# Optimization experiments

Measured on AMD Instinct MI355X. Metric: run time of the kernel, lower is better.

Reference implementation:

```python
import jax, jax.numpy as jnp
import numpy as np
import math

H = 256; W = 256
NUM_CURVES = 256
NUM_SAMPLES = 32
NUM_BEZIERS = 2
BDEG = 5            # Bernstein degree used by the module (bezier_degree+1)
CTRL_STRIDE = 5     # bezier_degree+1; segments share endpoints, wrap (closed curve)
N_CTRL = NUM_BEZIERS * CTRL_STRIDE   # 10 control points per closed curve
PIX_CHUNK = 512
CHOLESKY_BOUND = jnp.array([0.5, 0.0, 0.5], jnp.float32)


def _bernstein():
    # t in linspace(0.007, 0.993, S) exactly as _update_bernstein_cache
    t = jnp.linspace(0.007, 0.993, NUM_SAMPLES)
    i = jnp.arange(BDEG + 1, dtype=jnp.float32)
    comb = jnp.array([math.comb(BDEG, k) for k in range(BDEG + 1)], jnp.float32)
    return comb * (t[:, None] ** i) * ((1.0 - t[:, None]) ** (BDEG - i))  # [S, BDEG+1]


def _render(control_points, features_dc, cholesky, opacity, depth, background):
    Bmat = _bernstein()
    # closed curve: segment k uses control points (k*5 + j) mod 10, j=0..5
    seg_idx = (jnp.arange(NUM_BEZIERS)[:, None] * CTRL_STRIDE
               + jnp.arange(BDEG + 1)[None, :]) % N_CTRL          # [K, 6]
    seg_ctrl = control_points[:, seg_idx]                          # [N, K, 6, 2]
    pts = jnp.einsum('sj,nkjd->nksd', Bmat, seg_ctrl)              # [N, K, S, 2]
    pts = pts.reshape(NUM_CURVES, -1, 2)                           # [N, Gper, 2]
    gper = pts.shape[1]

    # normalized [-1,1] -> pixel coords
    means = (jnp.tanh(pts) * 0.5 + 0.5) * jnp.array([W, H], jnp.float32)
    means = means.reshape(-1, 2)                                   # [G, 2]

    # 2x2 covariance from lower-triangular Cholesky (per curve)
    c = cholesky + CHOLESKY_BOUND[None, :]                         # l11, l21, l22
    s00 = c[:, 0] ** 2
    s01 = c[:, 0] * c[:, 1]
    s11 = c[:, 1] ** 2 + c[:, 2] ** 2
    det = s00 * s11 - s01 ** 2
    conic = jnp.stack([s11 / det, -s01 / det, s00 / det], -1)      # [N, 3]

    rep = lambda a: jnp.repeat(a, gper, axis=0)
    conic_g = rep(conic)                                           # [G, 3]
    color_g = rep(jax.nn.sigmoid(features_dc))                     # [G, 3]
    alpha_g = rep(jax.nn.sigmoid(opacity))[:, 0]                   # [G]
    depth_g = rep(depth)[:, 0]                                     # [G]

    order = jnp.argsort(depth_g)                                   # front-to-back
    means_s = means[order]
    conic_s = conic_g[order]
    color_s = color_g[order]
    alpha_s = alpha_g[order]

    ys, xs = jnp.meshgrid(jnp.arange(H, dtype=jnp.float32) + 0.5,
                          jnp.arange(W, dtype=jnp.float32) + 0.5, indexing='ij')
    pix = jnp.stack([xs.ravel(), ys.ravel()], -1).reshape(-1, PIX_CHUNK, 2)

    @jax.checkpoint
    def render_chunk(p):                                           # [C,2] -> [C,3]
        dx = p[:, None, 0] - means_s[None, :, 0]
        dy = p[:, None, 1] - means_s[None, :, 1]
        power = (-0.5 * (conic_s[None, :, 0] * dx * dx
                         + conic_s[None, :, 2] * dy * dy)
                 - conic_s[None, :, 1] * dx * dy)
        a = jnp.clip(alpha_s[None, :] * jnp.exp(power), 0.0, 0.999)
        logT = jnp.cumsum(jnp.log1p(-a), axis=1)
        t_excl = jnp.exp(logT - jnp.log1p(-a))   # transmittance before each splat
        rgb = (a * t_excl) @ color_s             # [C, 3]
        return rgb + jnp.exp(logT[:, -1:]) * background[None, :]

    img = jax.lax.map(render_chunk, pix)                           # [P/C, C, 3]
    return jnp.clip(img.reshape(H, W, 3), 0.0, 1.0)


def setup_inputs() -> dict:
    key = jax.random.key(0)
    k1, k2, k3, k4 = jax.random.split(key, 4)
    return {
        "control_points": jax.random.normal(k1, (NUM_CURVES, N_CTRL, 2), jnp.float32),
        "features_dc": jax.random.uniform(k2, (NUM_CURVES, 3), jnp.float32),
        "cholesky": jax.random.uniform(k3, (NUM_CURVES, 3), jnp.float32),
        "opacity": jnp.ones((NUM_CURVES, 1), jnp.float32),
        "depth": jax.random.uniform(k4, (NUM_CURVES, 1), jnp.float32),
        "background": jnp.ones((3,), jnp.float32),
    }


def reference(control_points, features_dc, cholesky, opacity, depth, background):
    return _render(control_points, features_dc, cholesky, opacity, depth, background)
```

## Files before the change

### kernel.cpp

```cpp
#include <hip/hip_runtime.h>
#include <hip/hip_fp16.h>
#include <math.h>

#define NCURVES   256
#define GPER      64
#define NUM_G     (NCURVES*GPER)
#define IMG_W     256
#define IMG_H     256
#define TILE      8
#define TILES_X   (IMG_W/TILE)
#define TILES_Y   (IMG_H/TILE)
#define NTILES    (TILES_X*TILES_Y)
#define REC_F     8

#define A_MIN     3.0e-6f
#define P_CUT     (-12.6f)
#define T_EPS     1.0e-5f

#define WQ        4
#define GQ        (NUM_G/WQ)

__global__ __launch_bounds__(GPER)
void prep(const float* __restrict__ ctrl,
          const float* __restrict__ features,
          const float* __restrict__ cholesky,
          const float* __restrict__ opacity,
          const float* __restrict__ depth,
          float*       __restrict__ recs,
          unsigned*    __restrict__ bbox)
{
    int c   = blockIdx.x;
    int tid = threadIdx.x;

    float dc = depth[c];
    int r = 0;
    #pragma unroll
    for (int jj = 0; jj < 4; ++jj) {
        int j = tid + jj*64;
        float dj = depth[j];
        r += (dj < dc) || (dj == dc && j < c);
    }
    #pragma unroll
    for (int off = 32; off > 0; off >>= 1) r += __shfl_down(r, off, 64);
    r = __shfl(r, 0, 64);

    float c0 = cholesky[3*c+0] + 0.5f;
    float c1 = cholesky[3*c+1];
    float c2 = cholesky[3*c+2] + 0.5f;
    float s00 = c0*c0;
    float s01 = c0*c1;
    float s11 = c1*c1 + c2*c2;
    float inv = 1.0f / (s00*s11 - s01*s01);
    float A  =  s11*inv;
    float Bc = -s01*inv;
    float Cc =  s00*inv;

    float cr = 1.0f/(1.0f + __expf(-features[3*c+0]));
    float cg = 1.0f/(1.0f + __expf(-features[3*c+1]));
    float cb = 1.0f/(1.0f + __expf(-features[3*c+2]));
    float al = 1.0f/(1.0f + __expf(-opacity[c]));

    float cut = fmaxf(2.0f*(__logf(al) - __logf(A_MIN)), 0.0f);
    float rx = sqrtf(cut * s00);
    float ry = sqrtf(cut * s11);

    int k = tid >> 5;
    int s = tid & 31;
    float t = 0.007f + (float)s * (0.986f/31.0f);
    float u = 1.0f - t;
    float t2=t*t, t3=t2*t, t4=t3*t, t5=t4*t;
    float u2=u*u, u3=u2*u, u4=u3*u, u5=u4*u;
    float w[6] = { u5, 5.0f*t*u4, 10.0f*t2*u3, 10.0f*t3*u2, 5.0f*t4*u, t5 };

    const float* cp = ctrl + c*20;
    float px = 0.0f, py = 0.0f;
    #pragma unroll
    for (int j = 0; j < 6; ++j) {
        int idx = (k*5 + j) % 10;
        px += w[j]*cp[2*idx+0];
        py += w[j]*cp[2*idx+1];
    }
    float mx = (tanhf(px)*0.5f + 0.5f) * (float)IMG_W;
    float my = (tanhf(py)*0.5f + 0.5f) * (float)IMG_H;

    int gi = r*GPER + tid;

    unsigned rg  = (unsigned)__half_as_ushort(__float2half_rn(cr))
                 | ((unsigned)__half_as_ushort(__float2half_rn(cg)) << 16);
    unsigned cbp = (unsigned)__half_as_ushort(__float2half_rn(cb));

    float4* o4 = (float4*)(recs + (size_t)gi*REC_F);
    o4[0] = make_float4(mx, my, A, Bc);
    o4[1] = make_float4(Cc, al, __uint_as_float(rg), __uint_as_float(cbp));

    int tx0 = min(max((int)floorf((mx - rx) * (1.0f/TILE)), 0), TILES_X-1);
    int tx1 = min(max((int)floorf((mx + rx) * (1.0f/TILE)), 0), TILES_X-1);
    int ty0 = min(max((int)floorf((my - ry) * (1.0f/TILE)), 0), TILES_Y-1);
    int ty1 = min(max((int)floorf((my + ry) * (1.0f/TILE)), 0), TILES_Y-1);
    bbox[gi] = (unsigned)tx0 | ((unsigned)ty0<<8) | ((unsigned)tx1<<16) | ((unsigned)ty1<<24);
}

__global__ __launch_bounds__(256)
void render8x8(const float*    __restrict__ recs,
               const unsigned* __restrict__ bbox,
               const float*    __restrict__ background,
               float*          __restrict__ out)
{
    __shared__ unsigned short lst[WQ][GQ];
    __shared__ float4         pc[WQ][64];

    int tid   = threadIdx.x;
    int lane  = tid & 63;
    int w     = tid >> 6;
    int tile  = blockIdx.x;
    int tilex = tile & (TILES_X-1);
    int tiley = tile >> 5;
    unsigned long long lmask = (1ull << lane) - 1ull;

    int gb = w * GQ;

    int cnt = 0;
    #pragma unroll 1
    for (int b = 0; b < 8; ++b) {
        unsigned bb[8];
        #pragma unroll
        for (int u = 0; u < 8; ++u)
            bb[u] = bbox[gb + (b*8 + u)*64 + lane];
        #pragma unroll
        for (int u = 0; u < 8; ++u) {
            unsigned v = bb[u];
            bool pred = (tilex >= (int)( v        & 0xff)) &
                        (tilex <= (int)((v >> 16) & 0xff)) &
                        (tiley >= (int)((v >>  8) & 0xff)) &
                        (tiley <= (int)((v >> 24) & 0xff));
            unsigned long long m = __ballot(pred ? 1 : 0);
            if (pred)
                lst[w][cnt + (int)__popcll(m & lmask)] =
                    (unsigned short)((b*8 + u)*64 + lane);
            cnt += (int)__popcll(m);
        }
    }

    float pxf = (float)(tilex*TILE + (lane & 7)) + 0.5f;
    float pyf = (float)(tiley*TILE + (lane >> 3)) + 0.5f;

    float T = 1.0f, accr = 0.0f, accg = 0.0f, accb = 0.0f;

    #pragma unroll 2
    for (int j = 0; j < cnt; ++j) {
        int g = gb + (int)lst[w][j];
        const float4* rp = (const float4*)(recs + (size_t)g*REC_F);
        float4 r0 = rp[0];
        float4 r1 = rp[1];
        float dx = pxf - r0.x;
        float dy = pyf - r0.y;
        float p  = -0.5f*(r0.z*dx*dx + r1.x*dy*dy) - r0.w*dx*dy;
        if (p > P_CUT) {
            float a = fminf(r1.y * __expf(p), 0.999f);
            float wgt = a * T;
            unsigned rg = __float_as_uint(r1.z);
            accr += wgt * __half2float(__ushort_as_half((unsigned short)(rg & 0xffff)));
            accg += wgt * __half2float(__ushort_as_half((unsigned short)(rg >> 16)));
            accb += wgt * __half2float(__ushort_as_half((unsigned short)__float_as_uint(r1.w)));
            T *= (1.0f - a);
        }
        if (!__any(T > T_EPS)) break;
    }

    pc[w][lane] = make_float4(accr, accg, accb, T);
    __syncthreads();

    if (w == 0) {
        float4 a0 = pc[0][lane];
        float4 a1 = pc[1][lane];
        float4 a2 = pc[2][lane];
        float4 a3 = pc[3][lane];
        float r = a0.x + a0.w*(a1.x + a1.w*(a2.x + a2.w*a3.x));
        float g = a0.y + a0.w*(a1.y + a1.w*(a2.y + a2.w*a3.y));
        float b = a0.z + a0.w*(a1.z + a1.w*(a2.z + a2.w*a3.z));
        float Tt = a0.w * a1.w * a2.w * a3.w;

        r = fminf(fmaxf(r + Tt*background[0], 0.0f), 1.0f);
        g = fminf(fmaxf(g + Tt*background[1], 0.0f), 1.0f);
        b = fminf(fmaxf(b + Tt*background[2], 0.0f), 1.0f);

        int X = tilex*TILE + (lane & 7);
        int Y = tiley*TILE + (lane >> 3);
        size_t oi = ((size_t)Y*IMG_W + X)*3;
        out[oi+0] = r;
        out[oi+1] = g;
        out[oi+2] = b;
    }
}

extern "C" void kernel_launch(void* const* d_in, const int* in_sizes, int n_in,
                              void* d_out, int out_size, void* d_ws, size_t ws_size,
                              hipStream_t stream)
{
    const float* ctrl       = (const float*)d_in[0];
    const float* features   = (const float*)d_in[1];
    const float* cholesky   = (const float*)d_in[2];
    const float* opacity    = (const float*)d_in[3];
    const float* depth      = (const float*)d_in[4];
    const float* background = (const float*)d_in[5];
    float* out = (float*)d_out;

    char* w = (char*)d_ws;
    float*    recs  = (float*)   (w);
    unsigned* bboxp = (unsigned*)(w + 524288);

    prep<<<NCURVES, GPER, 0, stream>>>(ctrl, features, cholesky, opacity, depth,
                                       recs, bboxp);
    render8x8<<<NTILES, 256, 0, stream>>>(recs, bboxp, background, out);
}
```

Measured before the change: 95.28 us.

## Split depth range across eight wavefronts per tile and batch early-exit checks

After: 86.53 us. 9.2% less time.

```diff
diff --git a/kernel.cpp b/kernel.cpp
--- a/kernel.cpp
+++ b/kernel.cpp
@@ -17,8 +17,8 @@
 #define P_CUT     (-12.6f)
 #define T_EPS     1.0e-5f
 
-#define WQ        4
-#define GQ        (NUM_G/WQ)
+#define DW        8
+#define GSL       (NUM_G/DW)
 
 __global__ __launch_bounds__(GPER)
 void prep(const float* __restrict__ ctrl,
@@ -100,14 +100,16 @@
     bbox[gi] = (unsigned)tx0 | ((unsigned)ty0<<8) | ((unsigned)tx1<<16) | ((unsigned)ty1<<24);
 }
 
-__global__ __launch_bounds__(256)
-void render8x8(const float*    __restrict__ recs,
-               const unsigned* __restrict__ bbox,
-               const float*    __restrict__ background,
-               float*          __restrict__ out)
+__global__ __launch_bounds__(512)
+void render_tile8(const float*    __restrict__ recs,
+                  const unsigned* __restrict__ bbox,
+                  const float*    __restrict__ background,
+                  float*          __restrict__ out)
 {
-    __shared__ unsigned short lst[WQ][GQ];
-    __shared__ float4         pc[WQ][64];
+    __shared__ union {
+        unsigned short lst[DW][GSL];
+        float4         pc[DW][64];
+    } sh;
 
     int tid   = threadIdx.x;
     int lane  = tid & 63;
@@ -117,11 +119,11 @@
     int tiley = tile >> 5;
     unsigned long long lmask = (1ull << lane) - 1ull;
 
-    int gb = w * GQ;
+    int gb = w * GSL;
 
     int cnt = 0;
     #pragma unroll 1
-    for (int b = 0; b < 8; ++b) {
+    for (int b = 0; b < 4; ++b) {
         unsigned bb[8];
         #pragma unroll
         for (int u = 0; u < 8; ++u)
@@ -135,7 +137,7 @@
                         (tiley <= (int)((v >> 24) & 0xff));
             unsigned long long m = __ballot(pred ? 1 : 0);
             if (pred)
-                lst[w][cnt + (int)__popcll(m & lmask)] =
+                sh.lst[w][cnt + (int)__popcll(m & lmask)] =
                     (unsigned short)((b*8 + u)*64 + lane);
             cnt += (int)__popcll(m);
         }
@@ -146,40 +148,46 @@
 
     float T = 1.0f, accr = 0.0f, accg = 0.0f, accb = 0.0f;
 
-    #pragma unroll 2
-    for (int j = 0; j < cnt; ++j) {
-        int g = gb + (int)lst[w][j];
-        const float4* rp = (const float4*)(recs + (size_t)g*REC_F);
-        float4 r0 = rp[0];
-        float4 r1 = rp[1];
-        float dx = pxf - r0.x;
-        float dy = pyf - r0.y;
-        float p  = -0.5f*(r0.z*dx*dx + r1.x*dy*dy) - r0.w*dx*dy;
-        if (p > P_CUT) {
-            float a = fminf(r1.y * __expf(p), 0.999f);
-            float wgt = a * T;
-            unsigned rg = __float_as_uint(r1.z);
-            accr += wgt * __half2float(__ushort_as_half((unsigned short)(rg & 0xffff)));
-            accg += wgt * __half2float(__ushort_as_half((unsigned short)(rg >> 16)));
-            accb += wgt * __half2float(__ushort_as_half((unsigned short)__float_as_uint(r1.w)));
-            T *= (1.0f - a);
+    #pragma unroll 1
+    for (int jb = 0; jb < cnt; jb += 32) {
+        if (!__any(T > T_EPS)) break;
+        int je = jb + 32 < cnt ? jb + 32 : cnt;
+        #pragma unroll 4
+        for (int j = jb; j < je; ++j) {
+            int g = gb + (int)sh.lst[w][j];
+            const float4* rp = (const float4*)(recs + (size_t)g*REC_F);
+            float4 r0 = rp[0];
+            float4 r1 = rp[1];
+            float dx = pxf - r0.x;
+            float dy = pyf - r0.y;
+            float p  = -0.5f*(r0.z*dx*dx + r1.x*dy*dy) - r0.w*dx*dy;
+            if (p > P_CUT) {
+                float a = fminf(r1.y * __expf(p), 0.999f);
+                float wgt = a * T;
+                unsigned rg = __float_as_uint(r1.z);
+                accr += wgt * __half2float(__ushort_as_half((unsigned short)(rg & 0xffff)));
+                accg += wgt * __half2float(__ushort_as_half((unsigned short)(rg >> 16)));
+                accb += wgt * __half2float(__ushort_as_half((unsigned short)__float_as_uint(r1.w)));
+                T *= (1.0f - a);
+            }
         }
-        if (!__any(T > T_EPS)) break;
-    }
-
-    pc[w][lane] = make_float4(accr, accg, accb, T);
+    }
+
     __syncthreads();
+    sh.pc[w][lane] = make_float4(accr, accg, accb, T);
+    __syncthreads();
 
     if (w == 0) {
-        float4 a0 = pc[0][lane];
-        float4 a1 = pc[1][lane];
-        float4 a2 = pc[2][lane];
-        float4 a3 = pc[3][lane];
-        float r = a0.x + a0.w*(a1.x + a1.w*(a2.x + a2.w*a3.x));
-        float g = a0.y + a0.w*(a1.y + a1.w*(a2.y + a2.w*a3.y));
-        float b = a0.z + a0.w*(a1.z + a1.w*(a2.z + a2.w*a3.z));
-        float Tt = a0.w * a1.w * a2.w * a3.w;
-
+        float4 a = sh.pc[0][lane];
+        float r = a.x, g = a.y, b = a.z, Tt = a.w;
+        #pragma unroll
+        for (int s = 1; s < DW; ++s) {
+            float4 q = sh.pc[s][lane];
+            r  += Tt * q.x;
+            g  += Tt * q.y;
+            b  += Tt * q.z;
+            Tt *= q.w;
+        }
         r = fminf(fmaxf(r + Tt*background[0], 0.0f), 1.0f);
         g = fminf(fmaxf(g + Tt*background[1], 0.0f), 1.0f);
         b = fminf(fmaxf(b + Tt*background[2], 0.0f), 1.0f);
@@ -211,5 +219,5 @@
 
     prep<<<NCURVES, GPER, 0, stream>>>(ctrl, features, cholesky, opacity, depth,
                                        recs, bboxp);
-    render8x8<<<NTILES, 256, 0, stream>>>(recs, bboxp, background, out);
+    render_tile8<<<NTILES, 512, 0, stream>>>(recs, bboxp, background, out);
 }
```
